# Optimization experiments

Measured on AMD Instinct MI355X. Metric: run time of the kernel, lower is better.

The kernel has to match this reference:

```python
import jax, jax.numpy as jnp
import numpy as np

LMAX, MMAX = 6, 2
M_SIZE = (7, 6, 5)
SPHERE_C, HID = 128, 128
N_NODES, N_EDGES = 5000, 20000
N_COEFF_FULL = (LMAX + 1) ** 2                       # 49, l-primary node coeffs
N_COEFF_M = M_SIZE[0] + 2 * (M_SIZE[1] + M_SIZE[2])  # 29, m-primary edge coeffs
EXTRA_M0 = LMAX * HID                                # gate scalars from conv1


def _gate_idx():
    # maps each gated m-primary coefficient (all but l=0,m=0) to its degree index l-1
    idx = [l - 1 for l in range(1, LMAX + 1)]            # m=0 block (l=1..lmax)
    for m in range(1, MMAX + 1):
        for _ in range(2):                               # (-m, +m) components
            idx += [l - 1 for l in range(m, LMAX + 1)]
    return np.asarray(idx, dtype=np.int32)

GATE_IDX = jnp.asarray(_gate_idx())


def _layer_norm(h, s, b):
    mu = jnp.mean(h, axis=-1, keepdims=True)
    var = jnp.var(h, axis=-1, keepdims=True)
    return (h - mu) * jax.lax.rsqrt(var + 1e-5) * s + b


def _radial(e, w0, b0, s0, bb0, w1, b1, s1, bb1, w2, b2):
    h = jax.nn.silu(_layer_norm(e @ w0 + b0, s0, bb0))
    h = jax.nn.silu(_layer_norm(h @ w1 + b1, s1, bb1))
    return h @ w2 + b2


def _so2_conv(x, w_m0, b_m0, w_m1, w_m2, extra, x_rad=None):
    # x: [E, N_COEFF_M, C_in] in m-primary layout
    E = x.shape[0]
    w_m = (w_m1, w_m2)
    outs = []
    # m = 0: plain linear over flattened (l, channel)
    x0 = x[:, :M_SIZE[0]].reshape(E, -1)
    off_rad = 0
    if x_rad is not None:
        x0 = x0 * x_rad[:, :x0.shape[1]]
        off_rad = x0.shape[1]
    x0 = x0 @ w_m0 + b_m0
    x0_extra = None
    if extra:
        x0_extra, x0 = x0[:, :extra], x0[:, extra:]
    outs.append(x0.reshape(E, M_SIZE[0], -1))
    off = M_SIZE[0]
    # m > 0: complex-style SO(2) convolution per order m
    for m in range(1, MMAX + 1):
        sz = M_SIZE[m]
        xm = x[:, off:off + 2 * sz].reshape(E, 2, -1)    # [E, 2, sz*C_in]
        if x_rad is not None:
            d = xm.shape[2]
            xm = xm * x_rad[:, off_rad:off_rad + d][:, None, :]
            off_rad += d
        y = xm @ w_m[m - 1]                              # [E, 2, 2*sz*C_out]
        half = y.shape[2] // 2
        yr, yi = y[..., :half], y[..., half:]
        out_r = yr[:, 0] - yi[:, 1]
        out_i = yr[:, 1] + yi[:, 0]
        outs.append(jnp.stack((out_r, out_i), axis=1).reshape(E, 2 * sz, -1))
        off += 2 * sz
    out = jnp.concatenate(outs, axis=1)
    return (out, x0_extra) if extra else out


def _gate_act(gating, x):
    # gating: [E, LMAX*HID], x: [E, N_COEFF_M, HID]
    g = jax.nn.sigmoid(gating).reshape(-1, LMAX, HID)[:, GATE_IDX]  # [E, N_COEFF_M-1, HID]
    scalars = jax.nn.silu(x[:, :1])
    return jnp.concatenate((scalars, x[:, 1:] * g), axis=1)


def _edgewise(x, x_edge, edge_index, wig, wig_inv, env, params):
    (rw0, rb0, rs0, rbb0, rw1, rb1, rs1, rbb1, rw2, rb2,
     c1w0, c1b0, c1w1, c1w2, c2w0, c2b0, c2w1, c2w2) = params
    # gather source/target node features and concat channels -> [E, 49, 2C]
    msg = jnp.concatenate((x[edge_index[0]], x[edge_index[1]]), axis=2)
    # Wigner rotation + M mapping: l-primary (49) -> m-primary (29)
    msg = jnp.einsum('emj,ejc->emc', wig, msg)
    x_rad = _radial(x_edge, rw0, rb0, rs0, rbb0, rw1, rb1, rs1, rbb1, rw2, rb2)
    msg, gating = _so2_conv(msg, c1w0, c1b0, c1w1, c1w2, EXTRA_M0, x_rad)
    msg = _gate_act(gating, msg)
    msg = _so2_conv(msg, c2w0, c2b0, c2w1, c2w2, 0)
    msg = msg * env
    # inverse rotation: m-primary (29) -> l-primary (49)
    msg = jnp.einsum('ejm,emc->ejc', wig_inv, msg)
    return jax.ops.segment_sum(msg, edge_index[1], num_segments=x.shape[0])


def setup_inputs() -> dict:
    key = jax.random.key(0)
    ks = iter(jax.random.split(key, 40))
    def W(shape):
        return jax.random.normal(next(ks), shape, jnp.float32) / np.sqrt(shape[0])
    C_IN1 = 2 * SPHERE_C
    rad_out = C_IN1 * sum(M_SIZE)  # 4608
    inp = {}
    inp['x'] = jax.random.normal(next(ks), (N_NODES, N_COEFF_FULL, SPHERE_C), jnp.float32)
    inp['x_edge'] = jax.random.normal(next(ks), (N_EDGES, 128), jnp.float32)
    inp['edge_distance'] = jax.random.uniform(next(ks), (N_EDGES,), jnp.float32, 0.1, 6.0)
    inp['edge_index'] = jax.random.randint(next(ks), (2, N_EDGES), 0, N_NODES)
    inp['wigner_and_M_mapping'] = jax.random.normal(next(ks), (N_EDGES, N_COEFF_M, N_COEFF_FULL), jnp.float32) / np.sqrt(N_COEFF_FULL)
    inp['wigner_and_M_mapping_inv'] = jax.random.normal(next(ks), (N_EDGES, N_COEFF_FULL, N_COEFF_M), jnp.float32) / np.sqrt(N_COEFF_M)
    inp['edge_envelope'] = jax.random.uniform(next(ks), (N_EDGES, 1, 1), jnp.float32)
    inp['rad_w0'] = W((128, 256)); inp['rad_b0'] = jnp.zeros((256,), jnp.float32)
    inp['rad_ln0_s'] = jnp.ones((256,), jnp.float32); inp['rad_ln0_b'] = jnp.zeros((256,), jnp.float32)
    inp['rad_w1'] = W((256, 256)); inp['rad_b1'] = jnp.zeros((256,), jnp.float32)
    inp['rad_ln1_s'] = jnp.ones((256,), jnp.float32); inp['rad_ln1_b'] = jnp.zeros((256,), jnp.float32)
    inp['rad_w2'] = W((256, rad_out)); inp['rad_b2'] = jnp.zeros((rad_out,), jnp.float32)
    inp['c1_w_m0'] = W((M_SIZE[0] * C_IN1, M_SIZE[0] * HID + EXTRA_M0))
    inp['c1_b_m0'] = jnp.zeros((M_SIZE[0] * HID + EXTRA_M0,), jnp.float32)
    inp['c1_w_m1'] = W((M_SIZE[1] * C_IN1, 2 * M_SIZE[1] * HID))
    inp['c1_w_m2'] = W((M_SIZE[2] * C_IN1, 2 * M_SIZE[2] * HID))
    inp['c2_w_m0'] = W((M_SIZE[0] * HID, M_SIZE[0] * SPHERE_C))
    inp['c2_b_m0'] = jnp.zeros((M_SIZE[0] * SPHERE_C,), jnp.float32)
    inp['c2_w_m1'] = W((M_SIZE[1] * HID, 2 * M_SIZE[1] * SPHERE_C))
    inp['c2_w_m2'] = W((M_SIZE[2] * HID, 2 * M_SIZE[2] * SPHERE_C))
    return inp


def reference(x, x_edge, edge_distance, edge_index, wigner_and_M_mapping,
              wigner_and_M_mapping_inv, edge_envelope,
              rad_w0, rad_b0, rad_ln0_s, rad_ln0_b, rad_w1, rad_b1, rad_ln1_s, rad_ln1_b,
              rad_w2, rad_b2, c1_w_m0, c1_b_m0, c1_w_m1, c1_w_m2,
              c2_w_m0, c2_b_m0, c2_w_m1, c2_w_m2):
    # edge_distance is accepted (module signature) but unused in the original forward
    params = (rad_w0, rad_b0, rad_ln0_s, rad_ln0_b, rad_w1, rad_b1, rad_ln1_s, rad_ln1_b,
              rad_w2, rad_b2, c1_w_m0, c1_b_m0, c1_w_m1, c1_w_m2,
              c2_w_m0, c2_b_m0, c2_w_m1, c2_w_m2)
    return _edgewise(x, x_edge, edge_index, wigner_and_M_mapping,
                     wigner_and_M_mapping_inv, edge_envelope, params)
```

## Files before the change

### kernel.cpp

```cpp
#include <hip/hip_runtime.h>
#include <stdint.h>


#define E_NUM   20000
#define NN      5000

typedef uint16_t u16;
typedef __bf16  bf16x8 __attribute__((ext_vector_type(8)));
typedef float   f32x4  __attribute__((ext_vector_type(4)));
typedef uint16_t u16x8 __attribute__((ext_vector_type(8)));

__device__ __forceinline__ float bf2f(u16 h){
  uint32_t u = ((uint32_t)h) << 16;
  return __builtin_bit_cast(float, u);
}
__device__ __forceinline__ u16 f2bf(float f){
  uint32_t u = __builtin_bit_cast(uint32_t, f);
  u += 0x7fffu + ((u >> 16) & 1u);
  return (u16)(u >> 16);
}
__device__ __forceinline__ float sigm(float x){ return 1.f / (1.f + __expf(-x)); }

__device__ __forceinline__ void gload16(const void* g, void* l){
  __builtin_amdgcn_global_load_lds(
      (const __attribute__((address_space(1))) void*)g,
      (__attribute__((address_space(3))) void*)l, 16, 0, 0);
}

__device__ __forceinline__ int swz8(int orig, int nwg){
  int q = nwg >> 3, r = nwg & 7;
  int x = orig & 7, p = orig >> 3;
  int base = (x < r) ? x * (q + 1) : r * (q + 1) + (x - r) * q;
  return base + p;
}

__global__ void k_hist(const int* __restrict__ eidx, int* __restrict__ cnt){
  int e = blockIdx.x * 256 + threadIdx.x;
  if (e < E_NUM) atomicAdd(&cnt[eidx[E_NUM + e]], 1);
}
__global__ __launch_bounds__(256) void k_scan(const int* __restrict__ cnt,
                                              int* __restrict__ off){
  __shared__ int part[256];
  int t = threadIdx.x;
  int s = 0;
  #pragma unroll
  for (int i = 0; i < 20; ++i){
    int idx = t * 20 + i;
    if (idx < NN) s += cnt[idx];
  }
  part[t] = s;
  __syncthreads();
  if (t == 0){
    int run = 0;
    for (int i = 0; i < 256; ++i){ int v = part[i]; part[i] = run; run += v; }
  }
  __syncthreads();
  int run = part[t];
  #pragma unroll
  for (int i = 0; i < 20; ++i){
    int idx = t * 20 + i;
    if (idx < NN){ off[idx] = run; run += cnt[idx]; }
  }
}
__global__ void k_scatter(const int* __restrict__ eidx, int* __restrict__ off,
                          int* __restrict__ perm){
  int e = blockIdx.x * 256 + threadIdx.x;
  if (e < E_NUM){
    int pos = atomicAdd(&off[eidx[E_NUM + e]], 1);
    perm[pos] = e;
  }
}

__global__ void k_transpose_w(const float* __restrict__ in, u16* __restrict__ out,
                              int K, int N){
  __shared__ float t[32][33];
  int nb = blockIdx.x * 32, kb = blockIdx.y * 32;
  int tx = threadIdx.x & 31, ty = threadIdx.x >> 5;
  for (int i = ty; i < 32; i += 8)
    t[i][tx] = in[(size_t)(kb + i) * N + (nb + tx)];
  __syncthreads();
  for (int i = ty; i < 32; i += 8)
    out[(size_t)(nb + i) * K + (kb + tx)] = f2bf(t[tx][i]);
}

__global__ __launch_bounds__(256) void k_xpose(const float* __restrict__ x,
                                               u16* __restrict__ xT){
  __shared__ float t[6272];
  int n = blockIdx.x, tid = threadIdx.x;
  const float* xp = x + (size_t)n * 6272;
  for (int i = tid; i < 6272; i += 256) t[i] = xp[i];
  __syncthreads();
  int c = tid >> 1;
  int kh = (tid & 1) * 32;
  u16* o = xT + (size_t)n * 8192 + c * 64 + kh;
  #pragma unroll
  for (int q = 0; q < 4; ++q){
    u16x8 h;
    #pragma unroll
    for (int i = 0; i < 8; ++i){
      int k = kh + q * 8 + i;
      h[i] = (k < 49) ? f2bf(t[k * 128 + c]) : (u16)0;
    }
    *(u16x8*)(o + q * 8) = h;
  }
}

__global__ void k_gather_xe(const float* __restrict__ x_edge,
                            const int* __restrict__ perm,
                            u16* __restrict__ xe, int e0){
  int el = blockIdx.x, c = threadIdx.x;
  int pe = perm[e0 + el];
  xe[(size_t)el * 128 + c] = f2bf(x_edge[(size_t)pe * 128 + c]);
}

struct Seg {
  const u16* A; const u16* B; u16* C; const float* bias;
  int M, N, K, lda, blk0;
};
struct Seg5 { Seg s[5]; int nwg; };

__device__ __forceinline__ void gemm_tile(
    const u16* __restrict__ A, int lda, const u16* __restrict__ B,
    const float* __restrict__ bias, float* __restrict__ Cf,
    u16* __restrict__ Cb, int ldc, int M, int N, int K,
    int bm, int bn, u16* As , u16* Bs )
{
  const int tid  = threadIdx.x;
  const int lane = tid & 63;
  const int wave = tid >> 6;
  const int wm = wave >> 1, wn = wave & 1;
  const int fr = lane & 15, fq = lane >> 4;
  const int row0 = bm * 128;

  const int lr  = lane >> 2;
  const int lg  = lane & 3;
  const int rA0 = wave * 32 + lr;
  const int rA1 = rA0 + 16;
  const int g0  = lg ^ ((rA0 >> 1) & 3);
  const int g1  = lg ^ ((rA1 >> 1) & 3);
  int gra0 = row0 + rA0; if (gra0 > M - 1) gra0 = M - 1;
  int gra1 = row0 + rA1; if (gra1 > M - 1) gra1 = M - 1;
  const u16* aS0 = A + (size_t)gra0 * lda + g0 * 8;
  const u16* aS1 = A + (size_t)gra1 * lda + g1 * 8;
  const u16* bS0 = B + (size_t)(bn * 128 + rA0) * K + g0 * 8;
  const u16* bS1 = B + (size_t)(bn * 128 + rA1) * K + g1 * 8;
  const int dA0 = (wave * 32) * 32;
  const int dA1 = (wave * 32 + 16) * 32;

  int aoff[4], boff[4];
  #pragma unroll
  for (int mi = 0; mi < 4; ++mi){
    int r = wm * 64 + mi * 16 + fr;
    aoff[mi] = r * 32 + (fq ^ ((r >> 1) & 3)) * 8;
  }
  #pragma unroll
  for (int ni = 0; ni < 4; ++ni){
    int r = wn * 64 + ni * 16 + fr;
    boff[ni] = r * 32 + (fq ^ ((r >> 1) & 3)) * 8;
  }

  f32x4 acc[4][4];
  #pragma unroll
  for (int i = 0; i < 4; ++i)
    #pragma unroll
    for (int j = 0; j < 4; ++j) acc[i][j] = (f32x4){0.f, 0.f, 0.f, 0.f};

  auto stage = [&](int buf, int k0){
    gload16(aS0 + k0, &As[buf * 4096 + dA0]);
    gload16(aS1 + k0, &As[buf * 4096 + dA1]);
    gload16(bS0 + k0, &Bs[buf * 4096 + dA0]);
    gload16(bS1 + k0, &Bs[buf * 4096 + dA1]);
  };

  stage(0, 0);
  __syncthreads();
  int cur = 0;
  for (int k0 = 0; k0 < K; k0 += 32){
    if (k0 + 32 < K) stage(cur ^ 1, k0 + 32);
    bf16x8 af[4], bfv[4];
    #pragma unroll
    for (int mi = 0; mi < 4; ++mi)
      af[mi] = __builtin_bit_cast(bf16x8, *(const u16x8*)&As[cur * 4096 + aoff[mi]]);
    #pragma unroll
    for (int ni = 0; ni < 4; ++ni)
      bfv[ni] = __builtin_bit_cast(bf16x8, *(const u16x8*)&Bs[cur * 4096 + boff[ni]]);
    #pragma unroll
    for (int mi = 0; mi < 4; ++mi)
      #pragma unroll
      for (int ni = 0; ni < 4; ++ni)
        acc[mi][ni] = __builtin_amdgcn_mfma_f32_16x16x32_bf16(af[mi], bfv[ni], acc[mi][ni], 0, 0, 0);
    __syncthreads();
    cur ^= 1;
  }

  #pragma unroll
  for (int ni = 0; ni < 4; ++ni){
    int col = bn * 128 + wn * 64 + ni * 16 + fr;
    float bv = bias ? bias[col] : 0.f;
    #pragma unroll
    for (int mi = 0; mi < 4; ++mi){
      #pragma unroll
      for (int i = 0; i < 4; ++i){
        int row = row0 + wm * 64 + mi * 16 + fq * 4 + i;
        if (row < M){
          float v = acc[mi][ni][i] + bv;
          if (Cb) Cb[(size_t)row * ldc + col] = f2bf(v);
          else    Cf[(size_t)row * ldc + col] = v;
        }
      }
    }
  }
}

__global__ __launch_bounds__(256) void k_gemm_bt(
    const u16* __restrict__ A, int lda, const u16* __restrict__ B,
    const float* __restrict__ bias, float* __restrict__ Cf,
    u16* __restrict__ Cb, int ldc, int M, int N, int K)
{
  __shared__ u16 As[2 * 4096];
  __shared__ u16 Bs[2 * 4096];
  gemm_tile(A, lda, B, bias, Cf, Cb, ldc, M, N, K,
            blockIdx.y, blockIdx.x, As, Bs);
}

__global__ __launch_bounds__(256) void k_gemm_seg(Seg5 g)
{
  __shared__ u16 As[2 * 4096];
  __shared__ u16 Bs[2 * 4096];
  int wgid = swz8(blockIdx.x, g.nwg);
  Seg sg = g.s[4];
  if (wgid < g.s[4].blk0) sg = g.s[3];
  if (wgid < g.s[3].blk0) sg = g.s[2];
  if (wgid < g.s[2].blk0) sg = g.s[1];
  if (wgid < g.s[1].blk0) sg = g.s[0];
  int local = wgid - sg.blk0;
  int nbx = sg.N >> 7;
  int bn = local % nbx;
  int bm = local / nbx;
  gemm_tile(sg.A, sg.lda, sg.B, sg.bias, nullptr, sg.C, sg.N,
            sg.M, sg.N, sg.K, bm, bn, As, Bs);
}

__global__ __launch_bounds__(512) void k_gemm_ln(
    const u16* __restrict__ A, int lda, const u16* __restrict__ B ,
    const float* __restrict__ bias, const float* __restrict__ lns,
    const float* __restrict__ lnb, u16* __restrict__ out, int M, int K)
{
  __shared__ u16 As[2][4096];
  __shared__ u16 Bs[2][8192];
  __shared__ float rsum[128][4], rsq[128][4];
  const int tid = threadIdx.x, lane = tid & 63, w = tid >> 6;
  const int fr = lane & 15, fq = lane >> 4;
  const int bm = blockIdx.x, row0 = bm * 128;

  const int lr = lane >> 2, lg = lane & 3;
  int rA = w * 16 + lr;
  int gA = lg ^ ((rA >> 1) & 3);
  int grA = row0 + rA; if (grA > M - 1) grA = M - 1;
  const u16* aS = A + (size_t)grA * lda + gA * 8;
  int rB0 = w * 32 + lr, rB1 = rB0 + 16;
  int gB0 = lg ^ ((rB0 >> 1) & 3), gB1 = lg ^ ((rB1 >> 1) & 3);
  const u16* bS0 = B + (size_t)rB0 * K + gB0 * 8;
  const u16* bS1 = B + (size_t)rB1 * K + gB1 * 8;
  const int dA  = (w * 16) * 32;
  const int dB0 = (w * 32) * 32;
  const int dB1 = (w * 32 + 16) * 32;

  int aoff[4], boff[4];
  #pragma unroll
  for (int mi = 0; mi < 4; ++mi){
    int r = (w & 1) * 64 + mi * 16 + fr;
    aoff[mi] = r * 32 + (fq ^ ((r >> 1) & 3)) * 8;
  }
  #pragma unroll
  for (int ni = 0; ni < 4; ++ni){
    int ccol = (w >> 1) * 64 + ni * 16 + fr;
    boff[ni] = ccol * 32 + (fq ^ ((ccol >> 1) & 3)) * 8;
  }

  f32x4 acc[4][4];
  #pragma unroll
  for (int i = 0; i < 4; ++i)
    #pragma unroll
    for (int j = 0; j < 4; ++j) acc[i][j] = (f32x4){0.f, 0.f, 0.f, 0.f};

  auto stage = [&](int buf, int k0){
    gload16(aS + k0, &As[buf][dA]);
    gload16(bS0 + k0, &Bs[buf][dB0]);
    gload16(bS1 + k0, &Bs[buf][dB1]);
  };

  stage(0, 0);
  __syncthreads();
  int cur = 0;
  for (int k0 = 0; k0 < K; k0 += 32){
    if (k0 + 32 < K) stage(cur ^ 1, k0 + 32);
    bf16x8 af[4], bfv[4];
    #pragma unroll
    for (int mi = 0; mi < 4; ++mi)
      af[mi] = __builtin_bit_cast(bf16x8, *(const u16x8*)&As[cur][aoff[mi]]);
    #pragma unroll
    for (int ni = 0; ni < 4; ++ni)
      bfv[ni] = __builtin_bit_cast(bf16x8, *(const u16x8*)&Bs[cur][boff[ni]]);
    #pragma unroll
    for (int mi = 0; mi < 4; ++mi)
      #pragma unroll
      for (int ni = 0; ni < 4; ++ni)
        acc[mi][ni] = __builtin_amdgcn_mfma_f32_16x16x32_bf16(af[mi], bfv[ni], acc[mi][ni], 0, 0, 0);
    __syncthreads();
    cur ^= 1;
  }

  const int cq = w >> 1;
  float bv[4], sc[4], bb[4];
  #pragma unroll
  for (int ni = 0; ni < 4; ++ni){
    int col = cq * 64 + ni * 16 + fr;
    bv[ni] = bias[col]; sc[ni] = lns[col]; bb[ni] = lnb[col];
  }
  #pragma unroll
  for (int mi = 0; mi < 4; ++mi){
    #pragma unroll
    for (int i = 0; i < 4; ++i){
      float s1 = 0.f, s2 = 0.f;
      #pragma unroll
      for (int ni = 0; ni < 4; ++ni){
        float v = acc[mi][ni][i] + bv[ni];
        s1 += v; s2 += v * v;
      }
      #pragma unroll
      for (int off = 1; off < 16; off <<= 1){
        s1 += __shfl_xor(s1, off);
        s2 += __shfl_xor(s2, off);
      }
      if (fr == 0){
        int r = (w & 1) * 64 + mi * 16 + fq * 4 + i;
        rsum[r][cq] = s1; rsq[r][cq] = s2;
      }
    }
  }
  __syncthreads();
  #pragma unroll
  for (int mi = 0; mi < 4; ++mi){
    #pragma unroll
    for (int i = 0; i < 4; ++i){
      int r = (w & 1) * 64 + mi * 16 + fq * 4 + i;
      float S1 = rsum[r][0] + rsum[r][1] + rsum[r][2] + rsum[r][3];
      float S2 = rsq[r][0] + rsq[r][1] + rsq[r][2] + rsq[r][3];
      float mu  = S1 * (1.f / 256.f);
      float var = S2 * (1.f / 256.f) - mu * mu;
      float rs  = rsqrtf(var + 1e-5f);
      int row = row0 + r;
      if (row < M){
        #pragma unroll
        for (int ni = 0; ni < 4; ++ni){
          int col = cq * 64 + ni * 16 + fr;
          float nv = (acc[mi][ni][i] + bv[ni] - mu) * rs * sc[ni] + bb[ni];
          out[(size_t)row * 256 + col] = f2bf(nv * sigm(nv));
        }
      }
    }
  }
}

__global__ __launch_bounds__(256) void k_wig_fwd(
    const u16* __restrict__ xT, const int* __restrict__ eidx,
    const float* __restrict__ wig, const u16* __restrict__ xrad,
    u16* __restrict__ msgS, const int* __restrict__ perm, int e0)
{
  __shared__ u16 WL[32 * 64];
  int el = blockIdx.x, tid = threadIdx.x;
  int eg = perm[e0 + el];
  int lane = tid & 63, w = tid >> 6;

  const float* wp = wig + (size_t)eg * 1421;
  for (int idx = tid; idx < 2048; idx += 256){
    int m = idx >> 6, k = idx & 63;
    float v = (m < 29 && k < 49) ? wp[m * 49 + k] : 0.f;
    WL[m * 64 + ((((k >> 3) ^ (m & 7))) << 3) + (k & 7)] = f2bf(v);
  }

  const int fr = lane & 15, fq = lane >> 4;
  const int colbase = w * 64;
  int node = eidx[((w >> 1) ? E_NUM : 0) + eg];
  const u16* xb = xT + (size_t)node * 8192;
  bf16x8 bfv[4][2];
  #pragma unroll
  for (int ct = 0; ct < 4; ++ct)
    #pragma unroll
    for (int ks = 0; ks < 2; ++ks){
      int cc = ((w & 1) * 64) + ct * 16 + fr;
      bfv[ct][ks] = __builtin_bit_cast(bf16x8,
          *(const u16x8*)(xb + cc * 64 + (ks * 4 + fq) * 8));
    }
  __syncthreads();

  bf16x8 af[2][2];
  #pragma unroll
  for (int mt = 0; mt < 2; ++mt)
    #pragma unroll
    for (int ks = 0; ks < 2; ++ks){
      int m = mt * 16 + fr;
      int g = ks * 4 + fq;
      af[mt][ks] = __builtin_bit_cast(bf16x8,
          *(const u16x8*)&WL[m * 64 + ((g ^ (m & 7)) << 3)]);
    }
  f32x4 acc[2][4];
  #pragma unroll
  for (int mt = 0; mt < 2; ++mt)
    #pragma unroll
    for (int ct = 0; ct < 4; ++ct) acc[mt][ct] = (f32x4){0.f,0.f,0.f,0.f};
  #pragma unroll
  for (int mt = 0; mt < 2; ++mt)
    #pragma unroll
    for (int ct = 0; ct < 4; ++ct)
      #pragma unroll
      for (int ks = 0; ks < 2; ++ks)
        acc[mt][ct] = __builtin_amdgcn_mfma_f32_16x16x32_bf16(
            af[mt][ks], bfv[ct][ks], acc[mt][ct], 0, 0, 0);

  const u16* xr = xrad + (size_t)el * 4608;
  u16* o = msgS + (size_t)el * 7424;
  #pragma unroll
  for (int mt = 0; mt < 2; ++mt)
    #pragma unroll
    for (int ct = 0; ct < 4; ++ct){
      int col = colbase + ct * 16 + fr;
      #pragma unroll
      for (int r = 0; r < 4; ++r){
        int m = mt * 16 + fq * 4 + r;
        if (m < 29){
          int rr = (m < 13) ? m : (m < 24 ? m - 6 : m - 11);
          o[m * 256 + col] = f2bf(acc[mt][ct][r] * bf2f(xr[rr * 256 + col]));
        }
      }
    }
}

__global__ __launch_bounds__(256) void k_gate(
    const u16* __restrict__ c1m0, const u16* __restrict__ y10, const u16* __restrict__ y11,
    const u16* __restrict__ y20, const u16* __restrict__ y21, u16* __restrict__ msg2)
{
  int e = blockIdx.x, t = threadIdx.x;
  __shared__ float g[768];
  const u16* gp = c1m0 + (size_t)e * 1664;
  if (t < 96){
    u16x8 v = *(const u16x8*)(gp + t * 8);
    #pragma unroll
    for (int i = 0; i < 8; ++i) g[t * 8 + i] = sigm(bf2f(v[i]));
  }
  __syncthreads();
  const u16* x0 = gp + 768;
  const u16* a0 = y10 + (size_t)e * 1536;
  const u16* a1 = y11 + (size_t)e * 1536;
  const u16* b0 = y20 + (size_t)e * 1280;
  const u16* b1 = y21 + (size_t)e * 1280;
  u16* o = msg2 + (size_t)e * 3712;
  const int grp = (t & 15) * 8;
  for (int r = t >> 4; r < 29; r += 16){
    u16x8 outv;
    if (r == 0){
      u16x8 v = *(const u16x8*)(x0 + grp);
      #pragma unroll
      for (int i = 0; i < 8; ++i){ float f = bf2f(v[i]); outv[i] = f2bf(f * sigm(f)); }
    } else if (r < 7){
      u16x8 v = *(const u16x8*)(x0 + r * 128 + grp);
      #pragma unroll
      for (int i = 0; i < 8; ++i)
        outv[i] = f2bf(bf2f(v[i]) * g[(r - 1) * 128 + grp + i]);
    } else if (r < 19){
      int k = (r < 13) ? r - 7 : r - 13;
      u16x8 va = *(const u16x8*)(a0 + ((r < 13) ? k * 128 : 768 + k * 128) + grp);
      u16x8 vb = *(const u16x8*)(a1 + ((r < 13) ? 768 + k * 128 : k * 128) + grp);
      #pragma unroll
      for (int i = 0; i < 8; ++i){
        float fa = bf2f(va[i]), fb = bf2f(vb[i]);
        float val = (r < 13) ? (fa - fb) : (fb + fa);
        outv[i] = f2bf(val * g[k * 128 + grp + i]);
      }
    } else {
      int k = (r < 24) ? r - 19 : r - 24;
      u16x8 va = *(const u16x8*)(b0 + ((r < 24) ? k * 128 : 640 + k * 128) + grp);
      u16x8 vb = *(const u16x8*)(b1 + ((r < 24) ? 640 + k * 128 : k * 128) + grp);
      #pragma unroll
      for (int i = 0; i < 8; ++i){
        float fa = bf2f(va[i]), fb = bf2f(vb[i]);
        float val = (r < 24) ? (fa - fb) : (fb + fa);
        outv[i] = f2bf(val * g[(1 + k) * 128 + grp + i]);
      }
    }
    *(u16x8*)(o + r * 128 + grp) = outv;
  }
}

__global__ __launch_bounds__(128) void k_recomb2(
    const u16* __restrict__ m3x0, const u16* __restrict__ z10, const u16* __restrict__ z11,
    const u16* __restrict__ z20, const u16* __restrict__ z21, const float* __restrict__ env,
    u16* __restrict__ msg3T, const int* __restrict__ perm, int e0)
{
  __shared__ u16 s[6528];
  int e = blockIdx.x, c = threadIdx.x;
  {
    const u16* px0 = m3x0 + (size_t)e * 896;
    const u16* pa0 = z10 + (size_t)e * 1536;
    const u16* pa1 = z11 + (size_t)e * 1536;
    const u16* pb0 = z20 + (size_t)e * 1280;
    const u16* pb1 = z21 + (size_t)e * 1280;
    for (int v = c; v < 112; v += 128) *(u16x8*)(&s[v * 8])        = *(const u16x8*)(px0 + v * 8);
    for (int v = c; v < 192; v += 128) *(u16x8*)(&s[896 + v * 8])  = *(const u16x8*)(pa0 + v * 8);
    for (int v = c; v < 192; v += 128) *(u16x8*)(&s[2432 + v * 8]) = *(const u16x8*)(pa1 + v * 8);
    for (int v = c; v < 160; v += 128) *(u16x8*)(&s[3968 + v * 8]) = *(const u16x8*)(pb0 + v * 8);
    for (int v = c; v < 160; v += 128) *(u16x8*)(&s[5248 + v * 8]) = *(const u16x8*)(pb1 + v * 8);
  }
  __syncthreads();
  float ev = env[perm[e0 + e]];
  const u16* x0 = s;
  const u16* a0 = s + 896;
  const u16* a1 = s + 2432;
  const u16* b0 = s + 3968;
  const u16* b1 = s + 5248;
  u16 v[32];
  #pragma unroll
  for (int r = 0; r < 7; ++r) v[r] = f2bf(bf2f(x0[r * 128 + c]) * ev);
  #pragma unroll
  for (int k = 0; k < 6; ++k){
    float orr = bf2f(a0[k * 128 + c]) - bf2f(a1[768 + k * 128 + c]);
    float oii = bf2f(a1[k * 128 + c]) + bf2f(a0[768 + k * 128 + c]);
    v[7 + k]  = f2bf(orr * ev);
    v[13 + k] = f2bf(oii * ev);
  }
  #pragma unroll
  for (int k = 0; k < 5; ++k){
    float orr = bf2f(b0[k * 128 + c]) - bf2f(b1[640 + k * 128 + c]);
    float oii = bf2f(b1[k * 128 + c]) + bf2f(b0[640 + k * 128 + c]);
    v[19 + k] = f2bf(orr * ev);
    v[24 + k] = f2bf(oii * ev);
  }
  v[29] = 0; v[30] = 0; v[31] = 0;
  u16* o = msg3T + (size_t)e * 4096 + c * 32;
  #pragma unroll
  for (int q = 0; q < 4; ++q)
    *(u16x8*)(o + q * 8) = *(const u16x8*)(&v[q * 8]);
}

__global__ __launch_bounds__(256) void k_wig_inv(
    const u16* __restrict__ msg3T, const float* __restrict__ winv,
    const int* __restrict__ cnt, const int* __restrict__ soff,
    float* __restrict__ out, const int* __restrict__ perm, int e0, int cm)
{
  __shared__ u16 WV[2][2048];
  int d = blockIdx.x, tid = threadIdx.x;
  int cn = cnt[d];
  if (cn == 0) return;
  int runEnd = soff[d];
  int runStart = runEnd - cn;
  int start = runStart < e0 ? e0 : runStart;
  int end   = runEnd > e0 + cm ? e0 + cm : runEnd;
  if (start >= end) return;
  bool atom = (start != runStart) || (end != runEnd);

  int lane = tid & 63, w = tid >> 6;
  const int fr = lane & 15, fq = lane >> 4;
  const int jr = w * 16 + fr;

  auto stageW = [&](int buf, int pe){
    const float* wp = winv + (size_t)pe * 1421;
    for (int idx = tid; idx < 2048; idx += 256){
      int j = idx >> 5, m = idx & 31;
      float v = (j < 49 && m < 29) ? wp[j * 29 + m] : 0.f;
      WV[buf][j * 32 + (((m >> 3) ^ (j & 3)) << 3) + (m & 7)] = f2bf(v);
    }
  };

  f32x4 acc[8];
  #pragma unroll
  for (int ct = 0; ct < 8; ++ct) acc[ct] = (f32x4){0.f,0.f,0.f,0.f};

  stageW(0, perm[start]);
  __syncthreads();
  int b = 0;
  for (int t = start; t < end; ++t){
    if (t + 1 < end) stageW(b ^ 1, perm[t + 1]);
    bf16x8 a = __builtin_bit_cast(bf16x8,
        *(const u16x8*)&WV[b][jr * 32 + ((fq ^ (jr & 3)) << 3)]);
    const u16* bp = msg3T + (size_t)(t - e0) * 4096;
    #pragma unroll
    for (int ct = 0; ct < 8; ++ct){
      bf16x8 bo = __builtin_bit_cast(bf16x8,
          *(const u16x8*)(bp + (ct * 16 + fr) * 32 + fq * 8));
      acc[ct] = __builtin_amdgcn_mfma_f32_16x16x32_bf16(a, bo, acc[ct], 0, 0, 0);
    }
    __syncthreads();
    b ^= 1;
  }

  float* op = out + (size_t)d * 6272;
  if (atom){
    #pragma unroll
    for (int ct = 0; ct < 8; ++ct){
      int c = ct * 16 + fr;
      #pragma unroll
      for (int r = 0; r < 4; ++r){
        int j = w * 16 + fq * 4 + r;
        if (j < 49) atomicAdd(op + j * 128 + c, acc[ct][r]);
      }
    }
  } else {
    #pragma unroll
    for (int ct = 0; ct < 8; ++ct){
      int c = ct * 16 + fr;
      #pragma unroll
      for (int r = 0; r < 4; ++r){
        int j = w * 16 + fq * 4 + r;
        if (j < 49) op[j * 128 + c] = acc[ct][r];
      }
    }
  }
}

extern "C" void kernel_launch(void* const* d_in, const int* in_sizes, int n_in,
                              void* d_out, int out_size, void* d_ws, size_t ws_size,
                              hipStream_t stream)
{
  (void)in_sizes; (void)n_in;
  const float* x       = (const float*)d_in[0];
  const float* x_edge  = (const float*)d_in[1];
  const int*   eidx    = (const int*)d_in[3];
  const float* wig     = (const float*)d_in[4];
  const float* wig_inv = (const float*)d_in[5];
  const float* env     = (const float*)d_in[6];
  const float* rad_w0  = (const float*)d_in[7];
  const float* rad_b0  = (const float*)d_in[8];
  const float* ln0_s   = (const float*)d_in[9];
  const float* ln0_b   = (const float*)d_in[10];
  const float* rad_w1  = (const float*)d_in[11];
  const float* rad_b1  = (const float*)d_in[12];
  const float* ln1_s   = (const float*)d_in[13];
  const float* ln1_b   = (const float*)d_in[14];
  const float* rad_w2  = (const float*)d_in[15];
  const float* rad_b2  = (const float*)d_in[16];
  const float* c1w0    = (const float*)d_in[17];
  const float* c1b0    = (const float*)d_in[18];
  const float* c1w1    = (const float*)d_in[19];
  const float* c1w2    = (const float*)d_in[20];
  const float* c2w0    = (const float*)d_in[21];
  const float* c2b0    = (const float*)d_in[22];
  const float* c2w1    = (const float*)d_in[23];
  const float* c2w2    = (const float*)d_in[24];
  float* out = (float*)d_out;

  char* base = (char*)d_ws;
  size_t off = 0;
  auto alloc = [&](size_t bytes) -> char* {
    off = (off + 255) & ~(size_t)255;
    char* r = base + off;
    off += bytes;
    return r;
  };

  u16* wtR0  = (u16*)alloc((size_t)256  * 128  * 2);
  u16* wtR1  = (u16*)alloc((size_t)256  * 256  * 2);
  u16* wtR2  = (u16*)alloc((size_t)4608 * 256  * 2);
  u16* wtC10 = (u16*)alloc((size_t)1664 * 1792 * 2);
  u16* wtC11 = (u16*)alloc((size_t)1536 * 1536 * 2);
  u16* wtC12 = (u16*)alloc((size_t)1280 * 1280 * 2);
  u16* wtC20 = (u16*)alloc((size_t)896  * 896  * 2);
  u16* wtC21 = (u16*)alloc((size_t)1536 * 768  * 2);
  u16* wtC22 = (u16*)alloc((size_t)1280 * 640  * 2);
  u16* xT    = (u16*)alloc((size_t)NN * 8192 * 2);
  int* cnt   = (int*)alloc(NN * 4);
  int* soff  = (int*)alloc(NN * 4);
  int* perm  = (int*)alloc(E_NUM * 4);

  size_t fixed_end = (off + 65536) & ~(size_t)65535;
  size_t avail = (ws_size > fixed_end + (1u << 20)) ? (ws_size - fixed_end - (1u << 20)) : 0;
  long CH0 = (long)(avail / 40960);
  if (CH0 > E_NUM) CH0 = E_NUM;
  if (CH0 < 64) CH0 = 64;
  int nch = (int)((E_NUM + CH0 - 1) / CH0);
  int CH = (E_NUM + nch - 1) / nch;
  if (CH > CH0) CH = (int)CH0;

  off = fixed_end;
  const size_t C = (size_t)CH;
  u16*   xe   = (u16*)alloc(C * 128 * 2);
  u16*   h0   = (u16*)alloc(C * 256 * 2);
  u16*   h1   = (u16*)alloc(C * 256 * 2);
  u16* region1 = (u16*)alloc(C * 4608 * 2);
  u16* region2 = (u16*)alloc(C * 7424 * 2);
  u16* region3 = (u16*)alloc(C * 7296 * 2);
  u16* xrad = region1;
  u16* msg2 = region1;
  u16* msgS = region2;
  u16* m3x0 = region2;
  u16* z10  = region2 + C * 896;
  u16* z11  = region2 + C * 2432;
  u16* z20  = region2 + C * 3968;
  u16* z21  = region2 + C * 5248;
  u16* c1m0b = region3;
  u16* y10   = region3 + C * 1664;
  u16* y11   = region3 + C * 3200;
  u16* y20   = region3 + C * 4736;
  u16* y21   = region3 + C * 6016;
  u16* msg3T = region3;

  hipMemsetAsync(d_out, 0, (size_t)out_size * sizeof(float), stream);
  hipMemsetAsync(cnt, 0, NN * 4, stream);

  k_hist<<<(E_NUM + 255) / 256, 256, 0, stream>>>(eidx, cnt);
  k_scan<<<1, 256, 0, stream>>>(cnt, soff);
  k_scatter<<<(E_NUM + 255) / 256, 256, 0, stream>>>(eidx, soff, perm);
  k_xpose<<<NN, 256, 0, stream>>>(x, xT);

  auto tw = [&](const float* in, u16* o, int K, int N){
    k_transpose_w<<<dim3(N / 32, K / 32), 256, 0, stream>>>(in, o, K, N);
  };
  tw(rad_w0, wtR0, 128, 256);
  tw(rad_w1, wtR1, 256, 256);
  tw(rad_w2, wtR2, 256, 4608);
  tw(c1w0, wtC10, 1792, 1664);
  tw(c1w1, wtC11, 1536, 1536);
  tw(c1w2, wtC12, 1280, 1280);
  tw(c2w0, wtC20, 896, 896);
  tw(c2w1, wtC21, 768, 1536);
  tw(c2w2, wtC22, 640, 1280);

  for (int e0 = 0; e0 < E_NUM; e0 += CH){
    int cm = E_NUM - e0 < CH ? E_NUM - e0 : CH;
    int mb = (cm + 127) / 128;

    k_gather_xe<<<cm, 128, 0, stream>>>(x_edge, perm, xe, e0);

    k_gemm_ln<<<mb, 512, 0, stream>>>(xe, 128, wtR0, rad_b0, ln0_s, ln0_b, h0, cm, 128);
    k_gemm_ln<<<mb, 512, 0, stream>>>(h0, 256, wtR1, rad_b1, ln1_s, ln1_b, h1, cm, 256);
    k_gemm_bt<<<dim3(4608 / 128, mb), 256, 0, stream>>>(
        h1, 256, wtR2, rad_b2, nullptr, xrad, 4608, cm, 4608, 256);

    k_wig_fwd<<<cm, 256, 0, stream>>>(xT, eidx, wig, xrad, msgS, perm, e0);

    {
      Seg5 g;
      int b = 0;
      auto mk = [&](const u16* A, const u16* B, u16* Cb, const float* bias,
                    int N, int K) -> Seg {
        Seg s{A, B, Cb, bias, cm, N, K, 7424, b};
        b += (N >> 7) * mb;
        return s;
      };
      g.s[0] = mk(msgS,        wtC10, c1m0b, c1b0,   1664, 1792);
      g.s[1] = mk(msgS + 1792, wtC11, y10,   nullptr, 1536, 1536);
      g.s[2] = mk(msgS + 3328, wtC11, y11,   nullptr, 1536, 1536);
      g.s[3] = mk(msgS + 4864, wtC12, y20,   nullptr, 1280, 1280);
      g.s[4] = mk(msgS + 6144, wtC12, y21,   nullptr, 1280, 1280);
      g.nwg = b;
      k_gemm_seg<<<b, 256, 0, stream>>>(g);
    }

    k_gate<<<cm, 256, 0, stream>>>(c1m0b, y10, y11, y20, y21, msg2);

    {
      Seg5 g;
      int b = 0;
      auto mk = [&](const u16* A, const u16* B, u16* Cb, const float* bias,
                    int N, int K) -> Seg {
        Seg s{A, B, Cb, bias, cm, N, K, 3712, b};
        b += (N >> 7) * mb;
        return s;
      };
      g.s[0] = mk(msg2,        wtC20, m3x0, c2b0,   896,  896);
      g.s[1] = mk(msg2 + 896,  wtC21, z10,  nullptr, 1536, 768);
      g.s[2] = mk(msg2 + 1664, wtC21, z11,  nullptr, 1536, 768);
      g.s[3] = mk(msg2 + 2432, wtC22, z20,  nullptr, 1280, 640);
      g.s[4] = mk(msg2 + 3072, wtC22, z21,  nullptr, 1280, 640);
      g.nwg = b;
      k_gemm_seg<<<b, 256, 0, stream>>>(g);
    }

    k_recomb2<<<cm, 128, 0, stream>>>(m3x0, z10, z11, z20, z21, env, msg3T, perm, e0);

    k_wig_inv<<<NN, 256, 0, stream>>>(msg3T, wig_inv, cnt, soff, out, perm, e0, cm);
  }
}
```

Baseline: 2.356 ms.

## Widen GEMM tiles to 128x256 with 512-thread workgroups and padded N

Replaces the 128x128 GEMM tile with a 128x256 tile run by 8 waves, so each A tile loaded into LDS is reused across twice as many output columns. The grouped conv GEMMs and the radial output GEMM switch to this tile. Segments whose N is not a multiple of 256 (1664 and 896) get their weight buffers padded to 1792 and 1024 and zero-filled at startup. Output strides and downstream indexing in the gate and recombination kernels change to match, at the cost of extra padded compute and doubled LDS for B.

```diff
diff --git a/kernel.cpp b/kernel.cpp
--- a/kernel.cpp
+++ b/kernel.cpp
@@ -83,6 +83,12 @@
     out[(size_t)(nb + i) * K + (kb + tx)] = f2bf(t[tx][i]);
 }
 
+__global__ void k_zero16(u16* __restrict__ p, int n){
+  int i = blockIdx.x * 256 + threadIdx.x;
+  int stride = gridDim.x * 256;
+  for (; i < n; i += stride) p[i] = 0;
+}
+
 __global__ __launch_bounds__(256) void k_xpose(const float* __restrict__ x,
                                                u16* __restrict__ xT){
   __shared__ float t[6272];
@@ -115,48 +121,43 @@
 
 struct Seg {
   const u16* A; const u16* B; u16* C; const float* bias;
-  int M, N, K, lda, blk0;
+  int M, N, K, lda, blk0, Nb;
 };
 struct Seg5 { Seg s[5]; int nwg; };
 
-__device__ __forceinline__ void gemm_tile(
+__device__ __forceinline__ void gemm_tile256(
     const u16* __restrict__ A, int lda, const u16* __restrict__ B,
-    const float* __restrict__ bias, float* __restrict__ Cf,
-    u16* __restrict__ Cb, int ldc, int M, int N, int K,
+    const float* __restrict__ bias, int Nb, u16* __restrict__ Cb,
+    float* __restrict__ Cf, int ldc, int M, int K,
     int bm, int bn, u16* As , u16* Bs )
 {
-  const int tid  = threadIdx.x;
-  const int lane = tid & 63;
-  const int wave = tid >> 6;
-  const int wm = wave >> 1, wn = wave & 1;
+  const int tid = threadIdx.x, lane = tid & 63, w = tid >> 6;
   const int fr = lane & 15, fq = lane >> 4;
-  const int row0 = bm * 128;
-
-  const int lr  = lane >> 2;
-  const int lg  = lane & 3;
-  const int rA0 = wave * 32 + lr;
-  const int rA1 = rA0 + 16;
-  const int g0  = lg ^ ((rA0 >> 1) & 3);
-  const int g1  = lg ^ ((rA1 >> 1) & 3);
-  int gra0 = row0 + rA0; if (gra0 > M - 1) gra0 = M - 1;
-  int gra1 = row0 + rA1; if (gra1 > M - 1) gra1 = M - 1;
-  const u16* aS0 = A + (size_t)gra0 * lda + g0 * 8;
-  const u16* aS1 = A + (size_t)gra1 * lda + g1 * 8;
-  const u16* bS0 = B + (size_t)(bn * 128 + rA0) * K + g0 * 8;
-  const u16* bS1 = B + (size_t)(bn * 128 + rA1) * K + g1 * 8;
-  const int dA0 = (wave * 32) * 32;
-  const int dA1 = (wave * 32 + 16) * 32;
+  const int row0 = bm * 128, col0 = bn * 256;
+
+  const int lr = lane >> 2, lg = lane & 3;
+  int rA = w * 16 + lr;
+  int gA = lg ^ ((rA >> 1) & 3);
+  int grA = row0 + rA; if (grA > M - 1) grA = M - 1;
+  const u16* aS = A + (size_t)grA * lda + gA * 8;
+  int rB0 = w * 32 + lr, rB1 = rB0 + 16;
+  int gB0 = lg ^ ((rB0 >> 1) & 3), gB1 = lg ^ ((rB1 >> 1) & 3);
+  const u16* bS0 = B + (size_t)(col0 + rB0) * K + gB0 * 8;
+  const u16* bS1 = B + (size_t)(col0 + rB1) * K + gB1 * 8;
+  const int dA  = (w * 16) * 32;
+  const int dB0 = (w * 32) * 32;
+  const int dB1 = (w * 32 + 16) * 32;
 
   int aoff[4], boff[4];
   #pragma unroll
   for (int mi = 0; mi < 4; ++mi){
-    int r = wm * 64 + mi * 16 + fr;
+    int r = (w & 1) * 64 + mi * 16 + fr;
     aoff[mi] = r * 32 + (fq ^ ((r >> 1) & 3)) * 8;
   }
   #pragma unroll
   for (int ni = 0; ni < 4; ++ni){
-    int r = wn * 64 + ni * 16 + fr;
-    boff[ni] = r * 32 + (fq ^ ((r >> 1) & 3)) * 8;
+    int cc = (w >> 1) * 64 + ni * 16 + fr;
+    boff[ni] = cc * 32 + (fq ^ ((cc >> 1) & 3)) * 8;
   }
 
   f32x4 acc[4][4];
@@ -166,10 +167,9 @@
     for (int j = 0; j < 4; ++j) acc[i][j] = (f32x4){0.f, 0.f, 0.f, 0.f};
 
   auto stage = [&](int buf, int k0){
-    gload16(aS0 + k0, &As[buf * 4096 + dA0]);
-    gload16(aS1 + k0, &As[buf * 4096 + dA1]);
-    gload16(bS0 + k0, &Bs[buf * 4096 + dA0]);
-    gload16(bS1 + k0, &Bs[buf * 4096 + dA1]);
+    gload16(aS + k0, &As[buf * 4096 + dA]);
+    gload16(bS0 + k0, &Bs[buf * 8192 + dB0]);
+    gload16(bS1 + k0, &Bs[buf * 8192 + dB1]);
   };
 
   stage(0, 0);
@@ -183,7 +183,7 @@
       af[mi] = __builtin_bit_cast(bf16x8, *(const u16x8*)&As[cur * 4096 + aoff[mi]]);
     #pragma unroll
     for (int ni = 0; ni < 4; ++ni)
-      bfv[ni] = __builtin_bit_cast(bf16x8, *(const u16x8*)&Bs[cur * 4096 + boff[ni]]);
+      bfv[ni] = __builtin_bit_cast(bf16x8, *(const u16x8*)&Bs[cur * 8192 + boff[ni]]);
     #pragma unroll
     for (int mi = 0; mi < 4; ++mi)
       #pragma unroll
@@ -195,13 +195,13 @@
 
   #pragma unroll
   for (int ni = 0; ni < 4; ++ni){
-    int col = bn * 128 + wn * 64 + ni * 16 + fr;
-    float bv = bias ? bias[col] : 0.f;
+    int col = col0 + (w >> 1) * 64 + ni * 16 + fr;
+    float bv = (bias && col < Nb) ? bias[col] : 0.f;
     #pragma unroll
     for (int mi = 0; mi < 4; ++mi){
       #pragma unroll
       for (int i = 0; i < 4; ++i){
-        int row = row0 + wm * 64 + mi * 16 + fq * 4 + i;
+        int row = row0 + (w & 1) * 64 + mi * 16 + fq * 4 + i;
         if (row < M){
           float v = acc[mi][ni][i] + bv;
           if (Cb) Cb[(size_t)row * ldc + col] = f2bf(v);
@@ -212,21 +212,21 @@
   }
 }
 
-__global__ __launch_bounds__(256) void k_gemm_bt(
+__global__ __launch_bounds__(512) void k_gemm_bt256(
     const u16* __restrict__ A, int lda, const u16* __restrict__ B,
-    const float* __restrict__ bias, float* __restrict__ Cf,
-    u16* __restrict__ Cb, int ldc, int M, int N, int K)
+    const float* __restrict__ bias, int Nb, float* __restrict__ Cf,
+    u16* __restrict__ Cb, int ldc, int M, int K)
 {
   __shared__ u16 As[2 * 4096];
-  __shared__ u16 Bs[2 * 4096];
-  gemm_tile(A, lda, B, bias, Cf, Cb, ldc, M, N, K,
-            blockIdx.y, blockIdx.x, As, Bs);
-}
-
-__global__ __launch_bounds__(256) void k_gemm_seg(Seg5 g)
+  __shared__ u16 Bs[2 * 8192];
+  gemm_tile256(A, lda, B, bias, Nb, Cb, Cf, ldc, M, K,
+               blockIdx.y, blockIdx.x, As, Bs);
+}
+
+__global__ __launch_bounds__(512) void k_gemm_seg(Seg5 g)
 {
   __shared__ u16 As[2 * 4096];
-  __shared__ u16 Bs[2 * 4096];
+  __shared__ u16 Bs[2 * 8192];
   int wgid = swz8(blockIdx.x, g.nwg);
   Seg sg = g.s[4];
   if (wgid < g.s[4].blk0) sg = g.s[3];
@@ -234,11 +234,11 @@
   if (wgid < g.s[2].blk0) sg = g.s[1];
   if (wgid < g.s[1].blk0) sg = g.s[0];
   int local = wgid - sg.blk0;
-  int nbx = sg.N >> 7;
+  int nbx = sg.N >> 8;
   int bn = local % nbx;
   int bm = local / nbx;
-  gemm_tile(sg.A, sg.lda, sg.B, sg.bias, nullptr, sg.C, sg.N,
-            sg.M, sg.N, sg.K, bm, bn, As, Bs);
+  gemm_tile256(sg.A, sg.lda, sg.B, sg.bias, sg.Nb, sg.C, nullptr, sg.N,
+               sg.M, sg.K, bm, bn, As, Bs);
 }
 
 __global__ __launch_bounds__(512) void k_gemm_ln(
@@ -443,7 +443,7 @@
 {
   int e = blockIdx.x, t = threadIdx.x;
   __shared__ float g[768];
-  const u16* gp = c1m0 + (size_t)e * 1664;
+  const u16* gp = c1m0 + (size_t)e * 1792;
   if (t < 96){
     u16x8 v = *(const u16x8*)(gp + t * 8);
     #pragma unroll
@@ -501,7 +501,7 @@
   __shared__ u16 s[6528];
   int e = blockIdx.x, c = threadIdx.x;
   {
-    const u16* px0 = m3x0 + (size_t)e * 896;
+    const u16* px0 = m3x0 + (size_t)e * 1024;
     const u16* pa0 = z10 + (size_t)e * 1536;
     const u16* pa1 = z11 + (size_t)e * 1536;
     const u16* pb0 = z20 + (size_t)e * 1280;
@@ -661,10 +661,10 @@
   u16* wtR0  = (u16*)alloc((size_t)256  * 128  * 2);
   u16* wtR1  = (u16*)alloc((size_t)256  * 256  * 2);
   u16* wtR2  = (u16*)alloc((size_t)4608 * 256  * 2);
-  u16* wtC10 = (u16*)alloc((size_t)1664 * 1792 * 2);
+  u16* wtC10 = (u16*)alloc((size_t)1792 * 1792 * 2);
   u16* wtC11 = (u16*)alloc((size_t)1536 * 1536 * 2);
   u16* wtC12 = (u16*)alloc((size_t)1280 * 1280 * 2);
-  u16* wtC20 = (u16*)alloc((size_t)896  * 896  * 2);
+  u16* wtC20 = (u16*)alloc((size_t)1024 * 896  * 2);
   u16* wtC21 = (u16*)alloc((size_t)1536 * 768  * 2);
   u16* wtC22 = (u16*)alloc((size_t)1280 * 640  * 2);
   u16* xT    = (u16*)alloc((size_t)NN * 8192 * 2);
@@ -688,24 +688,26 @@
   u16*   h1   = (u16*)alloc(C * 256 * 2);
   u16* region1 = (u16*)alloc(C * 4608 * 2);
   u16* region2 = (u16*)alloc(C * 7424 * 2);
-  u16* region3 = (u16*)alloc(C * 7296 * 2);
+  u16* region3 = (u16*)alloc(C * 7424 * 2);
   u16* xrad = region1;
   u16* msg2 = region1;
   u16* msgS = region2;
   u16* m3x0 = region2;
-  u16* z10  = region2 + C * 896;
-  u16* z11  = region2 + C * 2432;
-  u16* z20  = region2 + C * 3968;
-  u16* z21  = region2 + C * 5248;
+  u16* z10  = region2 + C * 1024;
+  u16* z11  = region2 + C * 2560;
+  u16* z20  = region2 + C * 4096;
+  u16* z21  = region2 + C * 5376;
   u16* c1m0b = region3;
-  u16* y10   = region3 + C * 1664;
-  u16* y11   = region3 + C * 3200;
-  u16* y20   = region3 + C * 4736;
-  u16* y21   = region3 + C * 6016;
+  u16* y10   = region3 + C * 1792;
+  u16* y11   = region3 + C * 3328;
+  u16* y20   = region3 + C * 4864;
+  u16* y21   = region3 + C * 6144;
   u16* msg3T = region3;
 
   hipMemsetAsync(d_out, 0, (size_t)out_size * sizeof(float), stream);
   hipMemsetAsync(cnt, 0, NN * 4, stream);
+  k_zero16<<<2048, 256, 0, stream>>>(wtC10, 1792 * 1792);
+  k_zero16<<<2048, 256, 0, stream>>>(wtC20, 1024 * 896);
 
   k_hist<<<(E_NUM + 255) / 256, 256, 0, stream>>>(eidx, cnt);
   k_scan<<<1, 256, 0, stream>>>(cnt, soff);
@@ -733,8 +735,8 @@
 
     k_gemm_ln<<<mb, 512, 0, stream>>>(xe, 128, wtR0, rad_b0, ln0_s, ln0_b, h0, cm, 128);
     k_gemm_ln<<<mb, 512, 0, stream>>>(h0, 256, wtR1, rad_b1, ln1_s, ln1_b, h1, cm, 256);
-    k_gemm_bt<<<dim3(4608 / 128, mb), 256, 0, stream>>>(
-        h1, 256, wtR2, rad_b2, nullptr, xrad, 4608, cm, 4608, 256);
+    k_gemm_bt256<<<dim3(4608 / 256, mb), 512, 0, stream>>>(
+        h1, 256, wtR2, rad_b2, 4608, nullptr, xrad, 4608, cm, 256);
 
     k_wig_fwd<<<cm, 256, 0, stream>>>(xT, eidx, wig, xrad, msgS, perm, e0);
 
@@ -742,18 +744,18 @@
       Seg5 g;
       int b = 0;
       auto mk = [&](const u16* A, const u16* B, u16* Cb, const float* bias,
-                    int N, int K) -> Seg {
-        Seg s{A, B, Cb, bias, cm, N, K, 7424, b};
-        b += (N >> 7) * mb;
+                    int N, int K, int Nb) -> Seg {
+        Seg s{A, B, Cb, bias, cm, N, K, 7424, b, Nb};
+        b += (N >> 8) * mb;
         return s;
       };
-      g.s[0] = mk(msgS,        wtC10, c1m0b, c1b0,   1664, 1792);
-      g.s[1] = mk(msgS + 1792, wtC11, y10,   nullptr, 1536, 1536);
-      g.s[2] = mk(msgS + 3328, wtC11, y11,   nullptr, 1536, 1536);
-      g.s[3] = mk(msgS + 4864, wtC12, y20,   nullptr, 1280, 1280);
-      g.s[4] = mk(msgS + 6144, wtC12, y21,   nullptr, 1280, 1280);
+      g.s[0] = mk(msgS,        wtC10, c1m0b, c1b0,   1792, 1792, 1664);
+      g.s[1] = mk(msgS + 1792, wtC11, y10,   nullptr, 1536, 1536, 0);
+      g.s[2] = mk(msgS + 3328, wtC11, y11,   nullptr, 1536, 1536, 0);
+      g.s[3] = mk(msgS + 4864, wtC12, y20,   nullptr, 1280, 1280, 0);
+      g.s[4] = mk(msgS + 6144, wtC12, y21,   nullptr, 1280, 1280, 0);
       g.nwg = b;
-      k_gemm_seg<<<b, 256, 0, stream>>>(g);
+      k_gemm_seg<<<b, 512, 0, stream>>>(g);
     }
 
     k_gate<<<cm, 256, 0, stream>>>(c1m0b, y10, y11, y20, y21, msg2);
@@ -762,18 +764,18 @@
       Seg5 g;
       int b = 0;
       auto mk = [&](const u16* A, const u16* B, u16* Cb, const float* bias,
-                    int N, int K) -> Seg {
-        Seg s{A, B, Cb, bias, cm, N, K, 3712, b};
-        b += (N >> 7) * mb;
+                    int N, int K, int Nb) -> Seg {
+        Seg s{A, B, Cb, bias, cm, N, K, 3712, b, Nb};
+        b += (N >> 8) * mb;
         return s;
       };
-      g.s[0] = mk(msg2,        wtC20, m3x0, c2b0,   896,  896);
-      g.s[1] = mk(msg2 + 896,  wtC21, z10,  nullptr, 1536, 768);
-      g.s[2] = mk(msg2 + 1664, wtC21, z11,  nullptr, 1536, 768);
-      g.s[3] = mk(msg2 + 2432, wtC22, z20,  nullptr, 1280, 640);
-      g.s[4] = mk(msg2 + 3072, wtC22, z21,  nullptr, 1280, 640);
+      g.s[0] = mk(msg2,        wtC20, m3x0, c2b0,   1024, 896, 896);
+      g.s[1] = mk(msg2 + 896,  wtC21, z10,  nullptr, 1536, 768, 0);
+      g.s[2] = mk(msg2 + 1664, wtC21, z11,  nullptr, 1536, 768, 0);
+      g.s[3] = mk(msg2 + 2432, wtC22, z20,  nullptr, 1280, 640, 0);
+      g.s[4] = mk(msg2 + 3072, wtC22, z21,  nullptr, 1280, 640, 0);
       g.nwg = b;
-      k_gemm_seg<<<b, 256, 0, stream>>>(g);
+      k_gemm_seg<<<b, 512, 0, stream>>>(g);
     }
 
     k_recomb2<<<cm, 128, 0, stream>>>(m3x0, z10, z11, z20, z21, env, msg3T, perm, e0);
```

New measurement: 2.304 ms. -2.2%, faster.
